# Kernel optimization log

Measured on AMD Instinct MI355X. Metric: run time of the kernel, lower is better.

## Reference

```python
import jax, jax.numpy as jnp
import numpy as np

B, S, A, E, H, V, P = 128, 256, 8, 300, 300, 50000, 3


def _gru(x, wih, whh, bih, bhh):
    """torch.nn.GRU (single layer, batch_first) with gate order r,z,n."""
    h0 = jnp.zeros((x.shape[0], whh.shape[1]), x.dtype)

    def step(h, xt):
        gi = xt @ wih.T + bih            # [B,3H]
        gh = h @ whh.T + bhh
        ir, iz, in_ = jnp.split(gi, 3, axis=-1)
        hr, hz, hn = jnp.split(gh, 3, axis=-1)
        r = jax.nn.sigmoid(ir + hr)
        z = jax.nn.sigmoid(iz + hz)
        n = jnp.tanh(in_ + r * hn)
        hnew = (1.0 - z) * n + z * h
        return hnew, hnew

    _, ys = jax.lax.scan(step, h0, jnp.swapaxes(x, 0, 1))  # scan over time
    return jnp.swapaxes(ys, 0, 1)                          # [B,S,H]


def setup_inputs() -> dict:
    key = jax.random.key(0)
    ks = jax.random.split(key, 16)
    rn = lambda k, shape, s=0.05: jax.random.normal(k, shape, jnp.float32) * s
    z = lambda *shape: jnp.zeros(shape, jnp.float32)
    return {
        "embed_table": rn(ks[0], (V, E), 1.0),
        "w1": rn(ks[1], (E, 3 * E)), "b1": z(E),
        "w2": rn(ks[2], (1, E)),
        "wm": rn(ks[3], (E, E)), "bm": z(E),
        "wd": rn(ks[4], (P, E)), "bd": z(P),
        "wih_l": rn(ks[5], (3 * H, E)), "whh_l": rn(ks[6], (3 * H, H)),
        "bih_l": z(3 * H), "bhh_l": z(3 * H),
        "wih_r": rn(ks[7], (3 * H, E)), "whh_r": rn(ks[8], (3 * H, H)),
        "bih_r": z(3 * H), "bhh_r": z(3 * H),
        "wml": rn(ks[9], (1, H)), "bml": z(1),
        "wmr": rn(ks[10], (1, H)), "bmr": z(1),
        # all token ids >= 1 so lengths are exactly the padded length (packing == identity)
        "text_raw_indices": jax.random.randint(ks[11], (B, S), 1, V),
        "aspect_indices": jax.random.randint(ks[12], (B, A), 1, V),
        "x_l": jax.random.randint(ks[13], (B, S), 1, V),
        "x_r": jax.random.randint(ks[14], (B, S), 1, V),
    }


def _forward(embed_table, w1, b1, w2, wm, bm, wd, bd,
             wih_l, whh_l, bih_l, bhh_l, wih_r, whh_r, bih_r, bhh_r,
             wml, bml, wmr, bmr, text, aspect, xl, xr):
    memory_len = jnp.sum(text != 0, -1)    # [B]
    aspect_len = jnp.sum(aspect != 0, -1)
    left_len = jnp.sum(xl != 0, -1)

    v_a = jnp.sum(embed_table[aspect], 1) / aspect_len[:, None].astype(jnp.float32)  # [B,E]
    memory = embed_table[text]             # [B,S,E]

    # ---- context attention (attention #1), fully vectorized ----
    ctx_l = _gru(embed_table[xl], wih_l, whh_l, bih_l, bhh_l)  # [B,S,H]
    ctx_r = _gru(embed_table[xr], wih_r, whh_r, bih_r, bhh_r)
    attn_l = jax.nn.sigmoid(jnp.einsum('bsh,h->bs', ctx_l, wml[0]) + bml[0]) + 0.5  # [B,S]
    attn_r = jax.nn.sigmoid(jnp.einsum('bsh,h->bs', ctx_r, wmr[0]) + bmr[0]) + 0.5

    idx = jnp.arange(S)[None, :]                      # [1,S]
    a_start = (left_len - aspect_len)[:, None]        # [B,1]
    a_end = left_len[:, None]
    # attn_r reversed over the first aspect_end positions: attn_rr[i,t] = attn_r[i, a_end-1-t]
    attn_rr = jnp.take_along_axis(attn_r, jnp.clip(a_end - 1 - idx, 0, S - 1), axis=1)
    # attn_l shifted by aspect_start: attn_ls[i,t] = attn_l[i, t - a_start]
    attn_ls = jnp.take_along_axis(attn_l, jnp.clip(idx - a_start, 0, S - 1), axis=1)
    w = jnp.where(idx < a_start, attn_rr,
                  jnp.where(idx < a_end, (attn_rr + attn_ls) * 0.5, attn_ls))
    w = jnp.where(idx < memory_len[:, None], w, 1.0)  # untouched past memory_len
    memory = memory * w[..., None]

    v_s = jnp.sum(memory, 1) / memory_len[:, None].astype(jnp.float32)  # [B,E]

    # ---- content attention (attention #2) ----
    feat = jnp.concatenate([memory,
                            jnp.broadcast_to(v_a[:, None, :], memory.shape),
                            jnp.broadcast_to(v_s[:, None, :], memory.shape)], -1)  # [B,S,3E]
    c = jnp.tanh(feat @ w1.T + b1) @ w2.T             # [B,S,1]
    alpha = jax.nn.softmax(c[..., 0], axis=1)         # [B,S]
    v_ts = jnp.einsum('bse,bs->be', memory, alpha)    # [B,E]

    v_ns = v_ts + v_s                                 # dropout is identity at eval
    v_ms = jnp.tanh(v_ns @ wm.T + bm)
    return jax.nn.softmax(v_ms @ wd.T + bd, axis=-1)  # [B,P]


def reference(embed_table, w1, b1, w2, wm, bm, wd, bd,
              wih_l, whh_l, bih_l, bhh_l, wih_r, whh_r, bih_r, bhh_r,
              wml, bml, wmr, bmr, text_raw_indices, aspect_indices, x_l, x_r):
    return _forward(embed_table, w1, b1, w2, wm, bm, wd, bd,
                    wih_l, whh_l, bih_l, bhh_l, wih_r, whh_r, bih_r, bhh_r,
                    wml, bml, wmr, bmr, text_raw_indices, aspect_indices, x_l, x_r)
```

## Files before the change

kernel.cpp:

```cpp
#include <hip/hip_runtime.h>
#include <hip/hip_bf16.h>
#include <math.h>

#define Bd 128
#define Sd 256
#define Ad 8
#define Ed 300
#define Hd 300
#define EP 320
#define Pd 3
#define UC 5
#define BG 8

typedef __attribute__((ext_vector_type(8))) short bfrag;
typedef __attribute__((ext_vector_type(4))) float f32x4;
typedef __attribute__((ext_vector_type(4))) int i32x4;

#define OFF_LENS   0u
#define OFF_FLAGS  4096u
#define OFF_VA     8192u
#define OFF_VS     172032u
#define OFF_U      335872u
#define OFF_C      892928u
#define OFF_HF     1024000u
#define OFF_PART   1351680u
#define OFF_WF     11837440u
#define OFF_W1B    14295040u
#define OFF_XF     14499840u
#define OFF_MEMW   14499840u
#define WS_NEEDED  56442880u

__device__ __forceinline__ unsigned short f2bf(float f) {
    __hip_bfloat16 h = __float2bfloat16(f);
    return *reinterpret_cast<unsigned short*>(&h);
}
__device__ __forceinline__ float bf2f(unsigned short u) {
    __hip_bfloat16 h = *reinterpret_cast<__hip_bfloat16*>(&u);
    return __bfloat162float(h);
}
__device__ __forceinline__ float sigm(float x) {
    return __builtin_amdgcn_rcpf(1.f + __expf(-x));
}
__device__ __forceinline__ float fast_tanh(float x) {
    x = fminf(fmaxf(x, -15.f), 15.f);
    float e = __expf(2.f * x);
    return (e - 1.f) * __builtin_amdgcn_rcpf(e + 1.f);
}

__device__ __forceinline__ bfrag l2_load16b(const void* p) {
    bfrag v;
    asm volatile("global_load_dwordx4 %0, %1, off sc0"
                 : "=v"(v) : "v"(p) : "memory");
    return v;
}
__device__ __forceinline__ void l2_store16(void* p, i32x4 v) {
    asm volatile("global_store_dwordx4 %0, %1, off sc0"
                 :: "v"(p), "v"(v) : "memory");
}

__global__ void k_prep(const float* __restrict__ embed, const int* __restrict__ xl,
                       const int* __restrict__ xr, unsigned short* __restrict__ XF,
                       const float* __restrict__ wih_l, const float* __restrict__ whh_l,
                       const float* __restrict__ wih_r, const float* __restrict__ whh_r,
                       unsigned short* __restrict__ WF) {
    if (blockIdx.x < 512) {
        int side = blockIdx.x >> 8;
        int t = blockIdx.x & 255;
        const int* xs = side ? xr : xl;
        __shared__ int rows_s[Bd];
        if (threadIdx.x < Bd) rows_s[threadIdx.x] = xs[threadIdx.x*Sd + t];
        __syncthreads();
        unsigned short* dst = XF + ((size_t)(side*Sd + t))*40960;
        for (int v8 = threadIdx.x; v8 < 5120; v8 += 256) {
            int idx = v8 << 3;
            int bt = idx / 5120;
            int r1 = idx - bt*5120;
            int kt = r1 >> 9;
            int r2 = r1 & 511;
            int lane = r2 >> 3;
            int b = bt*16 + (lane & 15);
            int kk = kt*32 + (lane >> 4)*8;
            const float* src = embed + (size_t)rows_s[b]*Ed + kk;
            unsigned short tmp[8];
            if (kk + 8 <= Ed) {
                f32x4 f0 = *(const f32x4*)(src);
                f32x4 f1 = *(const f32x4*)(src + 4);
                #pragma unroll
                for (int j = 0; j < 4; ++j) { tmp[j] = f2bf(f0[j]); tmp[4+j] = f2bf(f1[j]); }
            } else {
                #pragma unroll
                for (int j = 0; j < 8; ++j)
                    tmp[j] = (kk + j < Ed) ? f2bf(src[j]) : (unsigned short)0;
            }
            *(bfrag*)(dst + idx) = *(const bfrag*)tmp;
        }
    } else {
        int bid = blockIdx.x - 512;
        int side = bid / 120;
        int r = bid - side*120;
        int mat = r / 60; r -= mat*60;
        int g = r / 20;
        int ut = r - g*20;
        const float* W = mat ? (side ? whh_r : whh_l) : (side ? wih_r : wih_l);
        unsigned short* dst = WF + (size_t)bid*5120;
        for (int v8 = threadIdx.x; v8 < 640; v8 += 256) {
            int idx = v8 << 3;
            int kt = idx >> 9;
            int r2 = idx & 511;
            int lane = r2 >> 3;
            int unit = ut*16 + (lane & 15);
            int kk = kt*32 + (lane >> 4)*8;
            unsigned short tmp[8];
            if (unit < Hd && kk + 8 <= Ed) {
                const float* src = W + (size_t)(g*Hd + unit)*Ed + kk;
                f32x4 f0 = *(const f32x4*)(src);
                f32x4 f1 = *(const f32x4*)(src + 4);
                #pragma unroll
                for (int j = 0; j < 4; ++j) { tmp[j] = f2bf(f0[j]); tmp[4+j] = f2bf(f1[j]); }
            } else {
                #pragma unroll
                for (int j = 0; j < 8; ++j) {
                    float v = (unit < Hd && kk + j < Ed) ? W[(size_t)(g*Hd + unit)*Ed + kk + j] : 0.f;
                    tmp[j] = f2bf(v);
                }
            }
            *(bfrag*)(dst + idx) = *(const bfrag*)tmp;
        }
    }
}

__global__ __launch_bounds__(256, 1) void k_gru(
        const unsigned short* __restrict__ WF,
        const unsigned short* __restrict__ XF,
        const float* __restrict__ bih_l, const float* __restrict__ bhh_l,
        const float* __restrict__ bih_r, const float* __restrict__ bhh_r,
        const float* __restrict__ wml, const float* __restrict__ wmr,
        unsigned short* __restrict__ HF,
        float* __restrict__ part, int* __restrict__ flags,
        const float* __restrict__ embed, const int* __restrict__ text,
        const int* __restrict__ aspect, const int* __restrict__ xl,
        int* __restrict__ lens, float* __restrict__ va,
        const float* __restrict__ w1, unsigned short* __restrict__ w1b) {
    if (blockIdx.x >= 80) {
        int xb = blockIdx.x - 80;
        int t = threadIdx.x;
        if (xb < 128) {
            int b = xb;
            __shared__ int red[3];
            __shared__ int aidx[Ad];
            if (t < 3) red[t] = 0;
            __syncthreads();
            if (t < Sd) {
                if (text[b*Sd + t] != 0) atomicAdd(&red[0], 1);
                if (xl[b*Sd + t]  != 0) atomicAdd(&red[2], 1);
            }
            if (t < Ad) {
                aidx[t] = aspect[b*Ad + t];
                if (aidx[t] != 0) atomicAdd(&red[1], 1);
            }
            __syncthreads();
            if (t < 3) lens[b*4 + t] = red[t];
            float inv = 1.0f / (float)red[1];
            for (int e = t; e < EP; e += 256) {
                float s = 0.f;
                if (e < Ed) {
                    for (int a = 0; a < Ad; ++a) s += embed[(size_t)aidx[a]*Ed + e];
                }
                va[b*EP + e] = s * inv;
            }
        } else {
            for (int idx = (xb - 128)*256 + t; idx < EP*EP; idx += 48*256) {
                int e = idx / EP, k = idx - e*EP;
                float v = (e < Ed && k < Ed) ? w1[(size_t)e*900 + k] : 0.f;
                w1b[idx] = f2bf(v);
            }
        }
        return;
    }

    int bg = blockIdx.x & 7;
    int r8 = blockIdx.x >> 3;
    int side = r8 & 1;
    int uc = r8 >> 1;
    int tid = threadIdx.x;
    int w = tid >> 6, lane = tid & 63, ul = lane & 15, lq = lane >> 4;
    int utg = uc*4 + w;
    int u = utg*16 + ul;

    const float* bih = side ? bih_r : bih_l;
    const float* bhh = side ? bhh_r : bhh_l;
    const float* wmv = side ? wmr : wml;

    float bR=0.f, bZ=0.f, bNI=0.f, bNH=0.f, wml_r=0.f;
    if (u < Hd) {
        bR = bih[u] + bhh[u];
        bZ = bih[Hd+u] + bhh[Hd+u];
        bNI = bih[2*Hd+u];
        bNH = bhh[2*Hd+u];
        wml_r = wmv[u];
    }

    bfrag wI[3][10], wH[3][10];
    #pragma unroll
    for (int g = 0; g < 3; ++g) {
        const unsigned short* pI = WF + ((size_t)((side*2+0)*3+g)*20 + utg)*5120 + lane*8;
        const unsigned short* pH = WF + ((size_t)((side*2+1)*3+g)*20 + utg)*5120 + lane*8;
        #pragma unroll
        for (int kt = 0; kt < 10; ++kt) {
            wI[g][kt] = *(const bfrag*)(pI + kt*512);
            wH[g][kt] = *(const bfrag*)(pH + kt*512);
        }
    }

    __shared__ __align__(16) unsigned short hn_s[1024];
    int* flgL2 = flags + (side*8 + bg)*16;
    int* flgIC = flags + 512 + (side*8 + bg)*16;
    unsigned short* hfb = HF + (size_t)((side*8 + bg)*2)*5120;
    const unsigned short* xbase = XF + ((size_t)side*Sd*8 + bg)*5120 + lane*8;

    bfrag xA[10], xB[10];
    #pragma unroll
    for (int kt = 0; kt < 10; ++kt)
        xA[kt] = *(const bfrag*)(xbase + 0 + kt*512);

    float hreg[4] = {0.f,0.f,0.f,0.f};
    const f32x4 zero4 = {0.f,0.f,0.f,0.f};

#define GRU_STEP(T, XIN, XOUT) do {                                            \
    f32x4 aR = zero4, aZ = zero4, aNI = zero4, aNH = zero4;                    \
    _Pragma("unroll")                                                          \
    for (int kt = 0; kt < 10; ++kt) {                                          \
        aR  = __builtin_amdgcn_mfma_f32_16x16x32_bf16(XIN[kt], wI[0][kt], aR, 0,0,0); \
        aZ  = __builtin_amdgcn_mfma_f32_16x16x32_bf16(XIN[kt], wI[1][kt], aZ, 0,0,0); \
        aNI = __builtin_amdgcn_mfma_f32_16x16x32_bf16(XIN[kt], wI[2][kt], aNI, 0,0,0); \
    }                                                                          \
    if ((T) > 0) {                                                             \
        if (w == 0) {                                                          \
            int iters = 0;                                                     \
            while (true) {                                                     \
                int v = (T);                                                   \
                if (lane < 2*UC)                                               \
                    v = __hip_atomic_fetch_add(flgL2 + lane, 0, __ATOMIC_RELAXED, __HIP_MEMORY_SCOPE_WORKGROUP); \
                if (__all(v >= (T))) break;                                    \
                if (((++iters) & 63) == 0) {                                   \
                    int vv = (T);                                              \
                    if (lane < 2*UC)                                           \
                        vv = __hip_atomic_load(flgIC + lane, __ATOMIC_RELAXED, __HIP_MEMORY_SCOPE_AGENT); \
                    if (__all(vv >= (T))) break;                               \
                }                                                              \
            }                                                                  \
        }                                                                      \
        __syncthreads();                                                       \
    }                                                                          \
    asm volatile("" ::: "memory");                                             \
    const unsigned short* hg = hfb + (size_t)((T) & 1)*5120 + lane*8;          \
    bfrag hf[10];                                                              \
    _Pragma("unroll")                                                          \
    for (int kt = 0; kt < 10; ++kt)                                            \
        hf[kt] = l2_load16b(hg + kt*512);                                      \
    asm volatile("s_waitcnt vmcnt(0)" ::: "memory");                           \
    __builtin_amdgcn_sched_barrier(0);                                         \
    _Pragma("unroll")                                                          \
    for (int kt = 0; kt < 10; ++kt) {                                          \
        aR  = __builtin_amdgcn_mfma_f32_16x16x32_bf16(hf[kt], wH[0][kt], aR, 0,0,0); \
        aZ  = __builtin_amdgcn_mfma_f32_16x16x32_bf16(hf[kt], wH[1][kt], aZ, 0,0,0); \
        aNH = __builtin_amdgcn_mfma_f32_16x16x32_bf16(hf[kt], wH[2][kt], aNH, 0,0,0); \
    }                                                                          \
    {                                                                          \
        int u_local = w*16 + ul;                                               \
        int kt_l = u_local >> 5, ko = u_local & 31;                            \
        _Pragma("unroll")                                                      \
        for (int i = 0; i < 4; ++i) {                                          \
            float rr = sigm(aR[i] + bR);                                       \
            float zz = sigm(aZ[i] + bZ);                                       \
            float nn = fast_tanh(aNI[i] + bNI + rr*(aNH[i] + bNH));            \
            float hv = (1.f - zz)*nn + zz*hreg[i];                             \
            hreg[i] = hv;                                                      \
            int rrow = lq*4 + i;                                               \
            hn_s[kt_l*512 + (rrow + ((ko>>3)<<4))*8 + (ko&7)] = f2bf(hv);      \
        }                                                                      \
    }                                                                          \
    __syncthreads();           \
    if (w < 2) {                                                               \
        unsigned short* hd = hfb + (size_t)(((T)+1) & 1)*5120 + uc*1024;       \
        l2_store16(hd + (size_t)tid*8, ((const i32x4*)hn_s)[tid]);             \
        asm volatile("s_waitcnt vmcnt(0)" ::: "memory");                       \
        if (lane == 0 && (T) < Sd-1) {                                         \
            __hip_atomic_fetch_add(flgL2 + uc*2 + w, 1, __ATOMIC_RELAXED, __HIP_MEMORY_SCOPE_WORKGROUP); \
            __hip_atomic_store(flgIC + uc*2 + w, (T)+1, __ATOMIC_RELAXED, __HIP_MEMORY_SCOPE_AGENT); \
        }                                                                      \
    }                                                                          \
    {                                                                          \
        int tn = ((T)+1 < Sd) ? (T)+1 : Sd-1;                                  \
        const unsigned short* xp = xbase + (size_t)tn*40960;                   \
        _Pragma("unroll")                                                      \
        for (int kt = 0; kt < 10; ++kt)                                        \
            XOUT[kt] = *(const bfrag*)(xp + kt*512);                           \
    }                                                                          \
    _Pragma("unroll")                                                          \
    for (int i = 0; i < 4; ++i) {                                              \
        float pv = hreg[i] * wml_r;                                            \
        pv += __shfl_xor(pv, 1, 64);                                           \
        pv += __shfl_xor(pv, 2, 64);                                           \
        pv += __shfl_xor(pv, 4, 64);                                           \
        pv += __shfl_xor(pv, 8, 64);                                           \
        if (ul == 0)                                                           \
            part[((size_t)((((side*8+bg)*UC + uc)*4 + w)*16) + lq*4 + i)*Sd + (T)] = pv; \
    }                                                                          \
} while (0)

    #pragma unroll 1
    for (int tt = 0; tt < Sd; tt += 2) {
        GRU_STEP(tt,   xA, xB);
        GRU_STEP(tt+1, xB, xA);
    }
#undef GRU_STEP
}

__global__ void k_awu(const float* __restrict__ part, const float* __restrict__ bml,
                      const float* __restrict__ bmr, const float* __restrict__ embed,
                      const int* __restrict__ text, const int* __restrict__ lens,
                      const float* __restrict__ w1, const float* __restrict__ b1,
                      const float* __restrict__ va,
                      unsigned short* __restrict__ memw, float* __restrict__ vs,
                      float* __restrict__ u) {
    int b = blockIdx.x;
    int bg = b >> 4, r = b & 15;
    __shared__ float attl_s[Sd], attr_s[Sd];
    __shared__ float w_sh[Sd];
    __shared__ int text_s[Sd];
    __shared__ float va_s[EP], vs_s[EP];
    int t = threadIdx.x;

    if (t < Sd) {
        float sl = 0.f, sr = 0.f;
        for (int c = 0; c < UC*4; ++c) {
            sl += part[((size_t)(((0*8+bg)*UC*4 + c)*16) + r)*Sd + t];
            sr += part[((size_t)(((1*8+bg)*UC*4 + c)*16) + r)*Sd + t];
        }
        attl_s[t] = sigm(sl + bml[0]) + 0.5f;
        attr_s[t] = sigm(sr + bmr[0]) + 0.5f;
        text_s[t] = text[b*Sd + t];
    }
    va_s[t] = va[b*EP + t];
    __syncthreads();

    int memlen = lens[b*4+0], asplen = lens[b*4+1], leftlen = lens[b*4+2];
    int a_start = leftlen - asplen, a_end = leftlen;
    if (t < Sd) {
        int i = t;
        int irr = a_end - 1 - i; irr = irr < 0 ? 0 : (irr > Sd-1 ? Sd-1 : irr);
        int ils = i - a_start;   ils = ils < 0 ? 0 : (ils > Sd-1 ? Sd-1 : ils);
        float arr_ = attr_s[irr], als = attl_s[ils];
        float w = (i < a_start) ? arr_ : ((i < a_end) ? 0.5f*(arr_+als) : als);
        if (i >= memlen) w = 1.0f;
        w_sh[i] = w;
    }
    __syncthreads();

    int e = t;
    float acc = 0.f;
    float invm = 1.0f/(float)memlen;
    for (int s = 0; s < Sd; ++s) {
        float v = (e < Ed) ? embed[(size_t)text_s[s]*Ed + e] : 0.f;
        float mw = v * w_sh[s];
        memw[((size_t)b*Sd + s)*EP + e] = f2bf(mw);
        acc += mw;
    }
    float vsv = acc * invm;
    vs[b*EP + e] = vsv;
    vs_s[e] = vsv;
    __syncthreads();

    float accu = 0.f;
    if (e < Ed) {
        accu = b1[e];
        const float* rw = w1 + (size_t)e*900;
        for (int k = 0; k < Ed; ++k) accu += va_s[k]*rw[300+k];
        for (int k = 0; k < Ed; ++k) accu += vs_s[k]*rw[600+k];
    }
    u[b*EP + e] = accu;
}

__global__ __launch_bounds__(256) void k_c(const unsigned short* __restrict__ memw,
                   const unsigned short* __restrict__ w1b,
                   const float* __restrict__ u, const float* __restrict__ w2,
                   float* __restrict__ cout) {
    int b = blockIdx.x >> 2;
    int s0 = (blockIdx.x & 3) * 64;
    __shared__ __align__(16) unsigned short A_s[64*328];
    __shared__ __align__(16) unsigned short Bp_s[EP*32];
    __shared__ float u_s[EP], w2_s[EP];
    for (int i = threadIdx.x; i < EP; i += 256) {
        u_s[i] = u[b*EP + i];
        w2_s[i] = (i < Ed) ? w2[i] : 0.f;
    }
    const unsigned short* Ag = memw + ((size_t)b*Sd + s0)*EP;
    for (int c8 = threadIdx.x; c8 < 64*40; c8 += 256) {
        int r = c8 / 40, kk = (c8 - r*40)*8;
        *(bfrag*)(A_s + r*328 + kk) = *(const bfrag*)(Ag + (size_t)r*EP + kk);
    }

    int wave = threadIdx.x >> 6, lane = threadIdx.x & 63;
    int ul = lane & 15, lq = lane >> 4;
    const f32x4 zero4 = {0.f,0.f,0.f,0.f};
    f32x4 acc[20];
    #pragma unroll
    for (int n = 0; n < 20; ++n) acc[n] = zero4;

    for (int kp = 0; kp < 10; ++kp) {
        __syncthreads();
        for (int c8 = threadIdx.x; c8 < EP*4; c8 += 256) {
            int e = c8 >> 2, kk = (c8 & 3)*8;
            *(bfrag*)(Bp_s + e*32 + kk) = *(const bfrag*)(w1b + (size_t)e*EP + kp*32 + kk);
        }
        __syncthreads();
        bfrag a = *(const bfrag*)(A_s + (wave*16 + ul)*328 + kp*32 + lq*8);
        #pragma unroll
        for (int n = 0; n < 20; ++n) {
            bfrag bb = *(const bfrag*)(Bp_s + (n*16 + ul)*32 + lq*8);
            acc[n] = __builtin_amdgcn_mfma_f32_16x16x32_bf16(a, bb, acc[n], 0, 0, 0);
        }
    }
    float cs[4] = {0.f,0.f,0.f,0.f};
    #pragma unroll
    for (int n = 0; n < 20; ++n) {
        int e = n*16 + ul;
        #pragma unroll
        for (int i = 0; i < 4; ++i)
            cs[i] += w2_s[e] * fast_tanh(acc[n][i] + u_s[e]);
    }
    #pragma unroll
    for (int i = 0; i < 4; ++i) {
        float v = cs[i];
        v += __shfl_xor(v, 1, 64); v += __shfl_xor(v, 2, 64);
        v += __shfl_xor(v, 4, 64); v += __shfl_xor(v, 8, 64);
        if (ul == 0) cout[(size_t)b*Sd + s0 + wave*16 + lq*4 + i] = v;
    }
}

__global__ void k_af(const float* __restrict__ cin, const unsigned short* __restrict__ memw,
                     const float* __restrict__ vs, const float* __restrict__ wm,
                     const float* __restrict__ bm, const float* __restrict__ wd,
                     const float* __restrict__ bd, float* __restrict__ out) {
    int b = blockIdx.x;
    int t = threadIdx.x;
    __shared__ float buf[Sd];
    __shared__ float al_s[Sd];
    __shared__ float vns_s[Ed];
    __shared__ float vms_s[Ed];
    __shared__ float lg_s[Pd];

    float v = 0.f;
    if (t < Sd) { v = cin[(size_t)b*Sd + t]; buf[t] = v; }
    __syncthreads();
    for (int s2 = 128; s2 > 0; s2 >>= 1) {
        if (t < s2) buf[t] = fmaxf(buf[t], buf[t+s2]);
        __syncthreads();
    }
    float mx = buf[0];
    __syncthreads();
    float ex = 0.f;
    if (t < Sd) { ex = __expf(v - mx); buf[t] = ex; }
    __syncthreads();
    for (int s2 = 128; s2 > 0; s2 >>= 1) {
        if (t < s2) buf[t] += buf[t+s2];
        __syncthreads();
    }
    if (t < Sd) al_s[t] = ex / buf[0];
    __syncthreads();

    int e = t;
    if (e < Ed) {
        float acc = 0.f;
        const unsigned short* mp = memw + (size_t)b*Sd*EP + e;
        for (int s = 0; s < Sd; ++s) acc += bf2f(mp[(size_t)s*EP]) * al_s[s];
        vns_s[e] = acc + vs[b*EP + e];
    }
    __syncthreads();
    if (e < Ed) {
        float acc = bm[e];
        const float* r = wm + (size_t)e*Ed;
        for (int k = 0; k < Ed; ++k) acc += vns_s[k]*r[k];
        vms_s[e] = fast_tanh(acc);
    }
    __syncthreads();
    if (e < Pd) {
        float acc = bd[e];
        const float* r = wd + (size_t)e*Ed;
        for (int k = 0; k < Ed; ++k) acc += vms_s[k]*r[k];
        lg_s[e] = acc;
    }
    __syncthreads();
    if (e < Pd) {
        float m = fmaxf(lg_s[0], fmaxf(lg_s[1], lg_s[2]));
        float den = __expf(lg_s[0]-m)+__expf(lg_s[1]-m)+__expf(lg_s[2]-m);
        out[b*Pd + e] = __expf(lg_s[e]-m)/den;
    }
}

extern "C" void kernel_launch(void* const* d_in, const int* in_sizes, int n_in,
                              void* d_out, int out_size, void* d_ws, size_t ws_size,
                              hipStream_t stream) {
    const float* embed = (const float*)d_in[0];
    const float* w1    = (const float*)d_in[1];
    const float* b1    = (const float*)d_in[2];
    const float* w2    = (const float*)d_in[3];
    const float* wm    = (const float*)d_in[4];
    const float* bm    = (const float*)d_in[5];
    const float* wd    = (const float*)d_in[6];
    const float* bd    = (const float*)d_in[7];
    const float* wih_l = (const float*)d_in[8];
    const float* whh_l = (const float*)d_in[9];
    const float* bih_l = (const float*)d_in[10];
    const float* bhh_l = (const float*)d_in[11];
    const float* wih_r = (const float*)d_in[12];
    const float* whh_r = (const float*)d_in[13];
    const float* bih_r = (const float*)d_in[14];
    const float* bhh_r = (const float*)d_in[15];
    const float* wml   = (const float*)d_in[16];
    const float* bml   = (const float*)d_in[17];
    const float* wmr   = (const float*)d_in[18];
    const float* bmr   = (const float*)d_in[19];
    const int* text    = (const int*)d_in[20];
    const int* aspect  = (const int*)d_in[21];
    const int* xl      = (const int*)d_in[22];
    const int* xr      = (const int*)d_in[23];

    if (ws_size < (size_t)WS_NEEDED) return;
    char* ws = (char*)d_ws;
    int* lens            = (int*)(ws + OFF_LENS);
    int* flags           = (int*)(ws + OFF_FLAGS);
    float* va            = (float*)(ws + OFF_VA);
    float* vs            = (float*)(ws + OFF_VS);
    float* u             = (float*)(ws + OFF_U);
    float* c             = (float*)(ws + OFF_C);
    unsigned short* HF   = (unsigned short*)(ws + OFF_HF);
    float* part          = (float*)(ws + OFF_PART);
    unsigned short* WF   = (unsigned short*)(ws + OFF_WF);
    unsigned short* w1b  = (unsigned short*)(ws + OFF_W1B);
    unsigned short* XF   = (unsigned short*)(ws + OFF_XF);
    unsigned short* memw = (unsigned short*)(ws + OFF_MEMW);

    hipMemsetAsync(ws + OFF_FLAGS, 0, 4096, stream);
    hipMemsetAsync(ws + OFF_HF, 0, 327680, stream);

    k_prep <<<752, 256, 0, stream>>>(embed, xl, xr, XF,
                                     wih_l, whh_l, wih_r, whh_r, WF);
    k_gru  <<<256, 256, 0, stream>>>(WF, XF, bih_l, bhh_l, bih_r, bhh_r,
                                     wml, wmr, HF, part, flags,
                                     embed, text, aspect, xl, lens, va, w1, w1b);
    k_awu  <<<128, 320, 0, stream>>>(part, bml, bmr, embed, text, lens,
                                     w1, b1, va, memw, vs, u);
    k_c    <<<512, 256, 0, stream>>>(memw, w1b, u, w2, c);
    k_af   <<<128, 320, 0, stream>>>(c, memw, vs, wm, bm, wd, bd, (float*)d_out);
}
```

Measured before the change: 782.2 us.

## Process two batch groups per GRU block to interleave recurrent chains

Each persistent GRU block now carries two independent batch-group recurrences instead of one. This halves the GRU blocks from 80 to 40 and the grid from 256 to 216. The input-gate MFMAs for both groups are issued up front, and the flag wait for one group's recurrent phase can overlap the other group's compute, hiding cross-block synchronization latency. The cost is a longer serial chain per block, since both phases run in sequence each step, plus more register pressure from doubled x fragments and hidden state.

```diff
diff --git a/kernel.cpp b/kernel.cpp
--- a/kernel.cpp
+++ b/kernel.cpp
@@ -141,8 +141,8 @@
         const int* __restrict__ aspect, const int* __restrict__ xl,
         int* __restrict__ lens, float* __restrict__ va,
         const float* __restrict__ w1, unsigned short* __restrict__ w1b) {
-    if (blockIdx.x >= 80) {
-        int xb = blockIdx.x - 80;
+    if (blockIdx.x >= 40) {
+        int xb = blockIdx.x - 40;
         int t = threadIdx.x;
         if (xb < 128) {
             int b = xb;
@@ -178,10 +178,11 @@
         return;
     }
 
-    int bg = blockIdx.x & 7;
-    int r8 = blockIdx.x >> 3;
-    int side = r8 & 1;
-    int uc = r8 >> 1;
+    int g8 = blockIdx.x & 7;
+    int uc = blockIdx.x >> 3;
+    int side = g8 >> 2;
+    int pr = g8 & 3;
+    int bg0 = pr*2, bg1 = pr*2 + 1;
     int tid = threadIdx.x;
     int w = tid >> 6, lane = tid & 63, ul = lane & 15, lq = lane >> 4;
     int utg = uc*4 + w;
@@ -212,40 +213,47 @@
         }
     }
 
-    __shared__ __align__(16) unsigned short hn_s[1024];
-    int* flgL2 = flags + (side*8 + bg)*16;
-    int* flgIC = flags + 512 + (side*8 + bg)*16;
-    unsigned short* hfb = HF + (size_t)((side*8 + bg)*2)*5120;
-    const unsigned short* xbase = XF + ((size_t)side*Sd*8 + bg)*5120 + lane*8;
-
-    bfrag xA[10], xB[10];
+    __shared__ __align__(16) unsigned short hn_s[2][1024];
+    int ci0 = side*8 + bg0, ci1 = side*8 + bg1;
+    int* flg0L2 = flags + ci0*16;            int* flg0IC = flags + 512 + ci0*16;
+    int* flg1L2 = flags + ci1*16;            int* flg1IC = flags + 512 + ci1*16;
+    unsigned short* hfb0 = HF + (size_t)(ci0*2)*5120;
+    unsigned short* hfb1 = HF + (size_t)(ci1*2)*5120;
+    const unsigned short* xb0 = XF + ((size_t)side*Sd*8 + bg0)*5120 + lane*8;
+    const unsigned short* xb1 = XF + ((size_t)side*Sd*8 + bg1)*5120 + lane*8;
+
+    bfrag x0[10], x1[10];
     #pragma unroll
-    for (int kt = 0; kt < 10; ++kt)
-        xA[kt] = *(const bfrag*)(xbase + 0 + kt*512);
-
-    float hreg[4] = {0.f,0.f,0.f,0.f};
+    for (int kt = 0; kt < 10; ++kt) {
+        x0[kt] = *(const bfrag*)(xb0 + kt*512);
+        x1[kt] = *(const bfrag*)(xb1 + kt*512);
+    }
+
+    float h0[4] = {0.f,0.f,0.f,0.f}, h1[4] = {0.f,0.f,0.f,0.f};
     const f32x4 zero4 = {0.f,0.f,0.f,0.f};
 
-#define GRU_STEP(T, XIN, XOUT) do {                                            \
-    f32x4 aR = zero4, aZ = zero4, aNI = zero4, aNH = zero4;                    \
+#define GRU_GI(XC, AR, AZ, ANI) do {                                           \
     _Pragma("unroll")                                                          \
     for (int kt = 0; kt < 10; ++kt) {                                          \
-        aR  = __builtin_amdgcn_mfma_f32_16x16x32_bf16(XIN[kt], wI[0][kt], aR, 0,0,0); \
-        aZ  = __builtin_amdgcn_mfma_f32_16x16x32_bf16(XIN[kt], wI[1][kt], aZ, 0,0,0); \
-        aNI = __builtin_amdgcn_mfma_f32_16x16x32_bf16(XIN[kt], wI[2][kt], aNI, 0,0,0); \
+        AR  = __builtin_amdgcn_mfma_f32_16x16x32_bf16(XC[kt], wI[0][kt], AR, 0,0,0); \
+        AZ  = __builtin_amdgcn_mfma_f32_16x16x32_bf16(XC[kt], wI[1][kt], AZ, 0,0,0); \
+        ANI = __builtin_amdgcn_mfma_f32_16x16x32_bf16(XC[kt], wI[2][kt], ANI, 0,0,0); \
     }                                                                          \
+} while (0)
+
+#define GRU_PHASE(T, C, HFB, FLGL2, FLGIC, HREG, AR, AZ, ANI, ANH, CI) do {    \
     if ((T) > 0) {                                                             \
-        if (w == 0) {                                                          \
+        if (w == 2*(C)) {                                                      \
             int iters = 0;                                                     \
             while (true) {                                                     \
                 int v = (T);                                                   \
                 if (lane < 2*UC)                                               \
-                    v = __hip_atomic_fetch_add(flgL2 + lane, 0, __ATOMIC_RELAXED, __HIP_MEMORY_SCOPE_WORKGROUP); \
+                    v = __hip_atomic_fetch_add((FLGL2) + lane, 0, __ATOMIC_RELAXED, __HIP_MEMORY_SCOPE_WORKGROUP); \
                 if (__all(v >= (T))) break;                                    \
                 if (((++iters) & 63) == 0) {                                   \
                     int vv = (T);                                              \
                     if (lane < 2*UC)                                           \
-                        vv = __hip_atomic_load(flgIC + lane, __ATOMIC_RELAXED, __HIP_MEMORY_SCOPE_AGENT); \
+                        vv = __hip_atomic_load((FLGIC) + lane, __ATOMIC_RELAXED, __HIP_MEMORY_SCOPE_AGENT); \
                     if (__all(vv >= (T))) break;                               \
                 }                                                              \
             }                                                                  \
@@ -253,68 +261,79 @@
         __syncthreads();                                                       \
     }                                                                          \
     asm volatile("" ::: "memory");                                             \
-    const unsigned short* hg = hfb + (size_t)((T) & 1)*5120 + lane*8;          \
-    bfrag hf[10];                                                              \
-    _Pragma("unroll")                                                          \
-    for (int kt = 0; kt < 10; ++kt)                                            \
-        hf[kt] = l2_load16b(hg + kt*512);                                      \
-    asm volatile("s_waitcnt vmcnt(0)" ::: "memory");                           \
-    __builtin_amdgcn_sched_barrier(0);                                         \
-    _Pragma("unroll")                                                          \
-    for (int kt = 0; kt < 10; ++kt) {                                          \
-        aR  = __builtin_amdgcn_mfma_f32_16x16x32_bf16(hf[kt], wH[0][kt], aR, 0,0,0); \
-        aZ  = __builtin_amdgcn_mfma_f32_16x16x32_bf16(hf[kt], wH[1][kt], aZ, 0,0,0); \
-        aNH = __builtin_amdgcn_mfma_f32_16x16x32_bf16(hf[kt], wH[2][kt], aNH, 0,0,0); \
+    {                                                                          \
+        const unsigned short* hg = (HFB) + (size_t)((T) & 1)*5120 + lane*8;    \
+        bfrag hf[10];                                                          \
+        _Pragma("unroll")                                                      \
+        for (int kt = 0; kt < 10; ++kt)                                        \
+            hf[kt] = l2_load16b(hg + kt*512);                                  \
+        asm volatile("s_waitcnt vmcnt(0)" ::: "memory");                       \
+        __builtin_amdgcn_sched_barrier(0);                                     \
+        _Pragma("unroll")                                                      \
+        for (int kt = 0; kt < 10; ++kt) {                                      \
+            AR  = __builtin_amdgcn_mfma_f32_16x16x32_bf16(hf[kt], wH[0][kt], AR, 0,0,0); \
+            AZ  = __builtin_amdgcn_mfma_f32_16x16x32_bf16(hf[kt], wH[1][kt], AZ, 0,0,0); \
+            ANH = __builtin_amdgcn_mfma_f32_16x16x32_bf16(hf[kt], wH[2][kt], ANH, 0,0,0); \
+        }                                                                      \
     }                                                                          \
     {                                                                          \
         int u_local = w*16 + ul;                                               \
         int kt_l = u_local >> 5, ko = u_local & 31;                            \
         _Pragma("unroll")                                                      \
         for (int i = 0; i < 4; ++i) {                                          \
-            float rr = sigm(aR[i] + bR);                                       \
-            float zz = sigm(aZ[i] + bZ);                                       \
-            float nn = fast_tanh(aNI[i] + bNI + rr*(aNH[i] + bNH));            \
-            float hv = (1.f - zz)*nn + zz*hreg[i];                             \
-            hreg[i] = hv;                                                      \
+            float rr = sigm(AR[i] + bR);                                       \
+            float zz = sigm(AZ[i] + bZ);                                       \
+            float nn = fast_tanh(ANI[i] + bNI + rr*(ANH[i] + bNH));            \
+            float hv = (1.f - zz)*nn + zz*HREG[i];                             \
+            HREG[i] = hv;                                                      \
             int rrow = lq*4 + i;                                               \
-            hn_s[kt_l*512 + (rrow + ((ko>>3)<<4))*8 + (ko&7)] = f2bf(hv);      \
+            hn_s[C][kt_l*512 + (rrow + ((ko>>3)<<4))*8 + (ko&7)] = f2bf(hv);   \
         }                                                                      \
     }                                                                          \
-    __syncthreads();           \
-    if (w < 2) {                                                               \
-        unsigned short* hd = hfb + (size_t)(((T)+1) & 1)*5120 + uc*1024;       \
-        l2_store16(hd + (size_t)tid*8, ((const i32x4*)hn_s)[tid]);             \
+    __syncthreads();        \
+    if ((w >> 1) == (C)) {                                                     \
+        unsigned short* hd = (HFB) + (size_t)(((T)+1) & 1)*5120 + uc*1024;     \
+        int sidx = (w & 1)*64 + lane;                                          \
+        l2_store16(hd + (size_t)sidx*8, ((const i32x4*)hn_s[C])[sidx]);        \
         asm volatile("s_waitcnt vmcnt(0)" ::: "memory");                       \
         if (lane == 0 && (T) < Sd-1) {                                         \
-            __hip_atomic_fetch_add(flgL2 + uc*2 + w, 1, __ATOMIC_RELAXED, __HIP_MEMORY_SCOPE_WORKGROUP); \
-            __hip_atomic_store(flgIC + uc*2 + w, (T)+1, __ATOMIC_RELAXED, __HIP_MEMORY_SCOPE_AGENT); \
+            __hip_atomic_fetch_add((FLGL2) + uc*2 + (w & 1), 1, __ATOMIC_RELAXED, __HIP_MEMORY_SCOPE_WORKGROUP); \
+            __hip_atomic_store((FLGIC) + uc*2 + (w & 1), (T)+1, __ATOMIC_RELAXED, __HIP_MEMORY_SCOPE_AGENT); \
         }                                                                      \
-    }                                                                          \
-    {                                                                          \
-        int tn = ((T)+1 < Sd) ? (T)+1 : Sd-1;                                  \
-        const unsigned short* xp = xbase + (size_t)tn*40960;                   \
-        _Pragma("unroll")                                                      \
-        for (int kt = 0; kt < 10; ++kt)                                        \
-            XOUT[kt] = *(const bfrag*)(xp + kt*512);                           \
     }                                                                          \
     _Pragma("unroll")                                                          \
     for (int i = 0; i < 4; ++i) {                                              \
-        float pv = hreg[i] * wml_r;                                            \
+        float pv = HREG[i] * wml_r;                                            \
         pv += __shfl_xor(pv, 1, 64);                                           \
         pv += __shfl_xor(pv, 2, 64);                                           \
         pv += __shfl_xor(pv, 4, 64);                                           \
         pv += __shfl_xor(pv, 8, 64);                                           \
         if (ul == 0)                                                           \
-            part[((size_t)((((side*8+bg)*UC + uc)*4 + w)*16) + lq*4 + i)*Sd + (T)] = pv; \
+            part[((size_t)(((CI)*UC + uc)*4 + w)*16 + lq*4 + i)*Sd + (T)] = pv; \
     }                                                                          \
 } while (0)
 
     #pragma unroll 1
-    for (int tt = 0; tt < Sd; tt += 2) {
-        GRU_STEP(tt,   xA, xB);
-        GRU_STEP(tt+1, xB, xA);
-    }
-#undef GRU_STEP
+    for (int t = 0; t < Sd; ++t) {
+        f32x4 aR0=zero4, aZ0=zero4, aNI0=zero4, aNH0=zero4;
+        f32x4 aR1=zero4, aZ1=zero4, aNI1=zero4, aNH1=zero4;
+        GRU_GI(x0, aR0, aZ0, aNI0);
+        GRU_GI(x1, aR1, aZ1, aNI1);
+        GRU_PHASE(t, 0, hfb0, flg0L2, flg0IC, h0, aR0, aZ0, aNI0, aNH0, ci0);
+        GRU_PHASE(t, 1, hfb1, flg1L2, flg1IC, h1, aR1, aZ1, aNI1, aNH1, ci1);
+        {
+            int tn = (t+1 < Sd) ? t+1 : Sd-1;
+            const unsigned short* xp0 = xb0 + (size_t)tn*40960;
+            const unsigned short* xp1 = xb1 + (size_t)tn*40960;
+            #pragma unroll
+            for (int kt = 0; kt < 10; ++kt) {
+                x0[kt] = *(const bfrag*)(xp0 + kt*512);
+                x1[kt] = *(const bfrag*)(xp1 + kt*512);
+            }
+        }
+    }
+#undef GRU_GI
+#undef GRU_PHASE
 }
 
 __global__ void k_awu(const float* __restrict__ part, const float* __restrict__ bml,
@@ -547,7 +566,7 @@
 
     k_prep <<<752, 256, 0, stream>>>(embed, xl, xr, XF,
                                      wih_l, whh_l, wih_r, whh_r, WF);
-    k_gru  <<<256, 256, 0, stream>>>(WF, XF, bih_l, bhh_l, bih_r, bhh_r,
+    k_gru  <<<216, 256, 0, stream>>>(WF, XF, bih_l, bhh_l, bih_r, bhh_r,
                                      wml, wmr, HF, part, flags,
                                      embed, text, aspect, xl, lens, va, w1, w1b);
     k_awu  <<<128, 320, 0, stream>>>(part, bml, bmr, embed, text, lens,
```

Result: slower. 2.207 ms (+182.2%).
